# Optimization experiments

Hardware: AMD Instinct MI355X
Metric: run time of the kernel (lower is better)

The kernel has to match this reference:

```python
import math
import jax, jax.numpy as jnp
import numpy as np

B, H, L = 8, 512, 4096
N = 64 // 2  # d_state//2 complex pairs
DT_MIN, DT_MAX = 1e-3, 0.1


def setup_inputs() -> dict:
    key = jax.random.key(0)
    k_u, k_dt, k_C, k_D, k_W = jax.random.split(key, 5)
    u = jax.random.normal(k_u, (B, H, L), dtype=jnp.float32)
    log_dt = jax.random.uniform(k_dt, (H,), dtype=jnp.float32) * (
        math.log(DT_MAX) - math.log(DT_MIN)) + math.log(DT_MIN)
    log_A_real = jnp.log(0.5 * jnp.ones((H, N), dtype=jnp.float32))
    A_imag = math.pi * jnp.broadcast_to(jnp.arange(N, dtype=jnp.float32), (H, N))
    C = jax.random.normal(k_C, (H, N, 2), dtype=jnp.float32)  # view_as_real of cfloat
    D = jax.random.normal(k_D, (H,), dtype=jnp.float32)
    W_out = jax.random.normal(k_W, (2 * H, H), dtype=jnp.float32) * 0.05  # 1x1 conv weight
    b_out = jnp.zeros((2 * H,), dtype=jnp.float32)
    return {"u": u, "log_dt": log_dt, "log_A_real": log_A_real, "A_imag": A_imag,
            "C": C, "D": D, "W_out": W_out, "b_out": b_out}


def _ssm_kernel(log_dt, log_A_real, A_imag, C, length):
    dt = jnp.exp(log_dt)                             # (H,)
    A = -jnp.exp(log_A_real) + 1j * A_imag           # (H,N) complex
    dtA = A * dt[:, None]                            # (H,N)
    l = jnp.arange(length, dtype=jnp.float32)
    K = jnp.exp(dtA[:, :, None] * l)                 # (H,N,L) complex Vandermonde
    Cc = C[..., 0] + 1j * C[..., 1]                  # (H,N)
    Cs = Cc * (jnp.exp(dtA) - 1.0) / A               # (H,N)
    return 2.0 * jnp.einsum('hn,hnl->hl', Cs, K).real  # (H,L) real kernel


def reference(u, log_dt, log_A_real, A_imag, C, D, W_out, b_out):
    length = u.shape[-1]
    k = _ssm_kernel(log_dt, log_A_real, A_imag, C, length)  # (H,L)
    n_fft = 2 * length
    k_f = jnp.fft.rfft(k, n=n_fft)                   # (H, L+1)
    u_f = jnp.fft.rfft(u, n=n_fft)                   # (B,H,L+1)
    y = jnp.fft.irfft(u_f * k_f, n=n_fft)[..., :length]  # FFT convolution
    y = y + u * D[:, None]                           # D skip connection
    y = jax.nn.gelu(y, approximate=False)            # torch nn.GELU = exact erf
    y = jnp.einsum('oh,bhl->bol', W_out, y) + b_out[:, None]  # 1x1 conv
    a, b = jnp.split(y, 2, axis=-2)                  # GLU over channel dim
    return a * jax.nn.sigmoid(b)
```

## Files before the change

### kernel.cpp

```cpp
#include <hip/hip_runtime.h>
#include <math.h>

constexpr int cB = 8, cH = 512, cL = 4096, cN = 32;
constexpr int cG = 32, cLC = 128;
constexpr int cHN = cH * cN;

constexpr size_t OF_RR  = 0;
constexpr size_t OF_RI  = (size_t)cHN;
constexpr size_t OF_RPR = (size_t)2*cHN;
constexpr size_t OF_RPI = (size_t)3*cHN;
constexpr size_t OF_C2R = (size_t)4*cHN;
constexpr size_t OF_C2I = (size_t)5*cHN;
constexpr size_t OF_DR  = (size_t)6*cHN;
constexpr size_t OF_DI  = (size_t)7*cHN;
constexpr size_t OF_K   = (size_t)8*cHN;
constexpr size_t OF_WP  = OF_K + (size_t)512*128;
constexpr size_t OF_A   = OF_WP + (size_t)1024*512/2;
constexpr size_t OF_V   = OF_A + (size_t)512*128*192/2;
constexpr size_t OF_XP  = OF_V + (size_t)512*64*128/2;
constexpr size_t OF_G   = OF_XP + (size_t)512*256*64/2;

typedef __bf16 bf16x8 __attribute__((ext_vector_type(8)));
typedef float  f32x4  __attribute__((ext_vector_type(4)));

static __device__ __forceinline__ ushort f2bf(float x) {
    unsigned u = __float_as_uint(x);
    unsigned r = (u + 0x7fffu + ((u >> 16) & 1u)) >> 16;
    return (ushort)r;
}
static __device__ __forceinline__ float bf2f(ushort v) {
    return __uint_as_float(((unsigned)v) << 16);
}
static __device__ __forceinline__ unsigned pk2(float a, float b) {
    return (unsigned)f2bf(a) | ((unsigned)f2bf(b) << 16);
}
static __device__ __forceinline__ float gelu(float v) {
    return 0.5f * v * (1.0f + erff(v * 0.70710678118654752f));
}

__global__ void k_consts(const float* __restrict__ log_dt,
                         const float* __restrict__ log_A_real,
                         const float* __restrict__ A_imag,
                         const float* __restrict__ Cin,
                         float* __restrict__ ws)
{
    int tid = blockIdx.x * 256 + threadIdx.x;
    if (tid >= cHN) return;
    int h = tid >> 5;
    float dt = expf(log_dt[h]);
    float Ar = -expf(log_A_real[tid]);
    float Ai = A_imag[tid];
    float dr = dt * Ar, di = dt * Ai;
    float er = expf(dr);
    float rr = er * cosf(di), ri = er * sinf(di);
    float erL = expf(dr * (float)cLC);
    float diL = di * (float)cLC;
    float rpr = erL * cosf(diL), rpi = erL * sinf(diL);
    float cr = Cin[2*tid], ci = Cin[2*tid+1];
    float nr = rr - 1.0f, ni = ri;
    float inv = 1.0f / (Ar*Ar + Ai*Ai);
    float wr = (nr*Ar + ni*Ai) * inv;
    float wi = (ni*Ar - nr*Ai) * inv;
    float csr = cr*wr - ci*wi;
    float csi = cr*wi + ci*wr;
    ws[OF_RR  + tid] = rr;  ws[OF_RI  + tid] = ri;
    ws[OF_RPR + tid] = rpr; ws[OF_RPI + tid] = rpi;
    ws[OF_C2R + tid] = 2.0f*csr; ws[OF_C2I + tid] = 2.0f*csi;
    ws[OF_DR  + tid] = dr;  ws[OF_DI  + tid] = di;
}

__global__ void k_pack_w(const float* __restrict__ W, ushort* __restrict__ Wp)
{
    int idx = blockIdx.x * 256 + threadIdx.x;
    int base = idx * 4;
    int m = base >> 9;
    int k = base & 511;
    int src = (m & 1) ? (512 + (m >> 1)) : (m >> 1);
    float4 v = *(const float4*)&W[(size_t)src * 512 + k];
    ushort4 o;
    o.x = f2bf(v.x); o.y = f2bf(v.y); o.z = f2bf(v.z); o.w = f2bf(v.w);
    *(ushort4*)&Wp[base] = o;
}

__global__ void k_vmat(const float* __restrict__ ws, ushort* __restrict__ wsu)
{
    int tid = blockIdx.x * 256 + threadIdx.x;
    int h = tid >> 5, n = tid & 31;
    float dr = ws[OF_DR + tid], di = ws[OF_DI + tid];
    float e127 = expf(dr * 127.f), a127 = di * 127.f;
    float pr = e127 * cosf(a127), pi_ = e127 * sinf(a127);
    float rie = expf(-dr);
    float rc = rie * cosf(di), rs = -rie * sinf(di);
    ushort* vre = wsu + 2*OF_V + ((size_t)h*64 + n) * 128;
    ushort* vim = wsu + 2*OF_V + ((size_t)h*64 + 32 + n) * 128;
    for (int j4 = 0; j4 < 128; j4 += 4) {
        ushort4 r4, i4;
        #pragma unroll
        for (int e = 0; e < 4; ++e) {
            ((ushort*)&r4)[e] = f2bf(pr);
            ((ushort*)&i4)[e] = f2bf(pi_);
            float npr = pr*rc - pi_*rs;
            float npi = pr*rs + pi_*rc;
            pr = npr; pi_ = npi;
        }
        *(ushort4*)&vre[j4] = r4;
        *(ushort4*)&vim[j4] = i4;
    }
}

__global__ void k_emat(const float* __restrict__ ws, float* __restrict__ wsf,
                       ushort* __restrict__ wsu)
{
    int tid = blockIdx.x * 256 + threadIdx.x;
    int h = tid >> 7, l = tid & 127;
    float fl = (float)l, fl1 = (float)(l + 1);
    const float* dr_ = ws + OF_DR + (size_t)h*32;
    const float* di_ = ws + OF_DI + (size_t)h*32;
    const float* c2r_ = ws + OF_C2R + (size_t)h*32;
    const float* c2i_ = ws + OF_C2I + (size_t)h*32;
    ushort* rowA = wsu + 2*OF_A + ((size_t)h*128 + l) * 192;
    float kacc = 0.f;
    for (int n4 = 0; n4 < 32; n4 += 4) {
        ushort4 prq, npq;
        #pragma unroll
        for (int e = 0; e < 4; ++e) {
            int n = n4 + e;
            float dr = dr_[n], di = di_[n], c2r = c2r_[n], c2i = c2i_[n];
            float e0 = expf(dr * fl), a0 = di * fl;
            float c0 = cosf(a0), s0 = sinf(a0);
            kacc += e0 * (c2r*c0 - c2i*s0);
            float e1 = expf(dr * fl1), a1 = di * fl1;
            float c1 = cosf(a1), s1 = sinf(a1);
            ((ushort*)&prq)[e] = f2bf(e1 * (c2r*c1 - c2i*s1));
            ((ushort*)&npq)[e] = f2bf(-e1 * (c2r*s1 + c2i*c1));
        }
        *(ushort4*)&rowA[128 + n4] = prq;
        *(ushort4*)&rowA[160 + n4] = npq;
    }
    wsf[OF_K + (size_t)h*128 + l] = kacc;
}

__global__ void k_build_T(const float* __restrict__ wsf, const float* __restrict__ Dvec,
                          ushort* __restrict__ wsu)
{
    __shared__ float kv[256];
    int t = threadIdx.x;
    int tid = blockIdx.x * 256 + t;
    int h = tid >> 7, l = tid & 127;
    kv[t] = wsf[OF_K + (size_t)blockIdx.x * 256 + t];
    __syncthreads();
    const float* krow = kv + ((t >> 7) << 7);
    float Dh = Dvec[h];
    ushort* row = wsu + 2*OF_A + ((size_t)h*128 + l) * 192;
    for (int j8 = 0; j8 < 128; j8 += 8) {
        uint4 q;
        unsigned w[4];
        #pragma unroll
        for (int p = 0; p < 4; ++p) {
            int j0 = j8 + 2*p, j1 = j0 + 1;
            float v0 = (j0 <= l) ? krow[l - j0] : 0.f;
            float v1 = (j1 <= l) ? krow[l - j1] : 0.f;
            if (j0 == l) v0 += Dh;
            if (j1 == l) v1 += Dh;
            w[p] = pk2(v0, v1);
        }
        q.x = w[0]; q.y = w[1]; q.z = w[2]; q.w = w[3];
        *(uint4*)&row[j8] = q;
    }
}

__global__ __launch_bounds__(256) void k_state_gemm(const float* __restrict__ u,
                                                    const ushort* __restrict__ wsu,
                                                    ushort* __restrict__ xp)
{
    __shared__ ushort Vs[64 * 136];
    __shared__ ushort Bs[256 * 40];
    const int t = threadIdx.x;
    const int h = blockIdx.x;
    const int wn = t >> 6, lane = t & 63;
    const int lm = lane & 15, q = lane >> 4;

    {
        int idx = t * 32;
        int row = idx >> 7, kk = idx & 127;
        const ushort* src = wsu + 2*OF_V + ((size_t)h*64 + row) * 128 + kk;
        uint4 v0 = *(const uint4*)&src[0],  v1 = *(const uint4*)&src[8];
        uint4 v2 = *(const uint4*)&src[16], v3 = *(const uint4*)&src[24];
        ushort* d = (ushort*)Vs + row * 136 + kk;
        *(uint4*)&d[0] = v0; *(uint4*)&d[8] = v1;
        *(uint4*)&d[16] = v2; *(uint4*)&d[24] = v3;
    }

    const int b = t >> 5, c = t & 31;
    f32x4 acc[4][4];
    #pragma unroll
    for (int i = 0; i < 4; ++i)
        #pragma unroll
        for (int j = 0; j < 4; ++j) acc[i][j] = (f32x4){0.f,0.f,0.f,0.f};

    for (int k0 = 0; k0 < 128; k0 += 32) {
        const float* up = u + ((size_t)(b*cH + h)) * cL + (size_t)c*128 + k0;
        float4 f[8];
        #pragma unroll
        for (int e = 0; e < 8; ++e) f[e] = *(const float4*)&up[4*e];
        __syncthreads();
        ushort* d = (ushort*)Bs + t * 40;
        #pragma unroll
        for (int e = 0; e < 4; ++e) {
            uint4 w;
            w.x = pk2(f[2*e].x, f[2*e].y);   w.y = pk2(f[2*e].z, f[2*e].w);
            w.z = pk2(f[2*e+1].x, f[2*e+1].y); w.w = pk2(f[2*e+1].z, f[2*e+1].w);
            *(uint4*)&d[8*e] = w;
        }
        __syncthreads();
        bf16x8 af[4], bfr[4];
        #pragma unroll
        for (int mi = 0; mi < 4; ++mi)
            af[mi] = *(const bf16x8*)&Vs[(16*mi + lm) * 136 + k0 + 8*q];
        #pragma unroll
        for (int ni = 0; ni < 4; ++ni)
            bfr[ni] = *(const bf16x8*)&Bs[(64*wn + 16*ni + lm) * 40 + 8*q];
        #pragma unroll
        for (int mi = 0; mi < 4; ++mi)
            #pragma unroll
            for (int ni = 0; ni < 4; ++ni)
                acc[mi][ni] = __builtin_amdgcn_mfma_f32_16x16x32_bf16(af[mi], bfr[ni], acc[mi][ni], 0,0,0);
    }
    #pragma unroll
    for (int mi = 0; mi < 4; ++mi)
        #pragma unroll
        for (int ni = 0; ni < 4; ++ni) {
            int col = 64*wn + 16*ni + lm;
            int comp = 16*mi + 4*q;
            ushort4 st;
            st.x = f2bf(acc[mi][ni][0]); st.y = f2bf(acc[mi][ni][1]);
            st.z = f2bf(acc[mi][ni][2]); st.w = f2bf(acc[mi][ni][3]);
            *(ushort4*)&xp[((size_t)h*256 + col) * 64 + comp] = st;
        }
}

__global__ __launch_bounds__(256) void k_scan2(const float* __restrict__ ws,
                                               ushort* __restrict__ xp)
{
    int tid = blockIdx.x * 256 + threadIdx.x;
    int n  = tid & 31;
    int bh = tid >> 5;
    int h  = bh & (cH - 1);
    int b  = bh >> 9;
    float rpr = ws[OF_RPR + (size_t)h*32 + n];
    float rpi = ws[OF_RPI + (size_t)h*32 + n];
    float Xr = 0.f, Xi = 0.f;
    ushort* base = xp + ((size_t)h*256 + (size_t)b*32) * 64 + n;
    for (int c = 0; c < cG; ++c) {
        ushort* p = base + (size_t)c * 64;
        float sr = bf2f(p[0]), si = bf2f(p[32]);
        p[0]  = f2bf(Xr);
        p[32] = f2bf(Xi);
        float nXr = fmaf(rpr, Xr, fmaf(-rpi, Xi, sr));
        float nXi = fmaf(rpr, Xi, fmaf(rpi, Xr, si));
        Xr = nXr; Xi = nXi;
    }
}

__global__ __launch_bounds__(256) void k_conv(const float* __restrict__ u,
                                              const ushort* __restrict__ wsu,
                                              ushort* __restrict__ g)
{
    __shared__ ushort As[128 * 40];
    __shared__ ushort Bs[128 * 40];
    const int t = threadIdx.x;
    const int ctile = blockIdx.x;
    const int h = blockIdx.y;
    const int wave = t >> 6, lane = t & 63;
    const int wm = wave & 1, wn = wave >> 1;
    const int lm = lane & 15, q = lane >> 4;

    const int arow = t & 127, ah = t >> 7;
    const int col = arow, half = ah;
    const int gc = ctile * 128 + col;
    const int ub = gc >> 5, uc = gc & 31;

    const ushort* Ab = wsu + 2*OF_A + ((size_t)h*128 + arow) * 192;
    const ushort* xpB = wsu + 2*OF_XP + ((size_t)h*256 + gc) * 64;

    f32x4 acc[4][4];
    #pragma unroll
    for (int i = 0; i < 4; ++i)
        #pragma unroll
        for (int j = 0; j < 4; ++j) acc[i][j] = (f32x4){0.f,0.f,0.f,0.f};

    for (int k0 = 0; k0 < 192; k0 += 32) {
        uint4 a0 = *(const uint4*)&Ab[k0 + 16*ah];
        uint4 a1 = *(const uint4*)&Ab[k0 + 16*ah + 8];
        uint4 b0, b1;
        if (k0 < 128) {
            const float* up = u + ((size_t)(ub*cH + h)) * cL + (size_t)uc*128 + k0 + 16*half;
            float4 f0 = *(const float4*)&up[0],  f1 = *(const float4*)&up[4];
            float4 f2 = *(const float4*)&up[8],  f3 = *(const float4*)&up[12];
            b0.x = pk2(f0.x,f0.y); b0.y = pk2(f0.z,f0.w);
            b0.z = pk2(f1.x,f1.y); b0.w = pk2(f1.z,f1.w);
            b1.x = pk2(f2.x,f2.y); b1.y = pk2(f2.z,f2.w);
            b1.z = pk2(f3.x,f3.y); b1.w = pk2(f3.z,f3.w);
        } else {
            const ushort* xs = xpB + (k0 - 128) + 16*half;
            b0 = *(const uint4*)&xs[0];
            b1 = *(const uint4*)&xs[8];
        }
        __syncthreads();
        *(uint4*)&As[arow*40 + 16*ah]     = a0;
        *(uint4*)&As[arow*40 + 16*ah + 8] = a1;
        *(uint4*)&Bs[col*40 + 16*half]     = b0;
        *(uint4*)&Bs[col*40 + 16*half + 8] = b1;
        __syncthreads();
        bool skip = (wm == 0) && (k0 == 64 || k0 == 96);
        if (!skip) {
            bf16x8 af[4], bfr[4];
            #pragma unroll
            for (int mi = 0; mi < 4; ++mi)
                af[mi] = *(const bf16x8*)&As[(64*wm + 16*mi + lm) * 40 + 8*q];
            #pragma unroll
            for (int ni = 0; ni < 4; ++ni)
                bfr[ni] = *(const bf16x8*)&Bs[(64*wn + 16*ni + lm) * 40 + 8*q];
            #pragma unroll
            for (int mi = 0; mi < 4; ++mi)
                #pragma unroll
                for (int ni = 0; ni < 4; ++ni)
                    acc[mi][ni] = __builtin_amdgcn_mfma_f32_16x16x32_bf16(af[mi], bfr[ni], acc[mi][ni], 0,0,0);
        }
    }
    #pragma unroll
    for (int ni = 0; ni < 4; ++ni) {
        int ocol = ctile*128 + 64*wn + 16*ni + lm;
        int ob = ocol >> 5, oc = ocol & 31;
        ushort* grow = g + ((size_t)(ob*cH + h)) * cL + (size_t)oc*128;
        #pragma unroll
        for (int mi = 0; mi < 4; ++mi) {
            int l = 64*wm + 16*mi + 4*q;
            ushort4 st;
            st.x = f2bf(gelu(acc[mi][ni][0]));
            st.y = f2bf(gelu(acc[mi][ni][1]));
            st.z = f2bf(gelu(acc[mi][ni][2]));
            st.w = f2bf(gelu(acc[mi][ni][3]));
            *(ushort4*)&grow[l] = st;
        }
    }
}

constexpr int LDK = 40;
__global__ __launch_bounds__(256) void k_gemm_mfma(const ushort* __restrict__ Wp,
                                                   const float* __restrict__ bias,
                                                   const ushort* __restrict__ gbf,
                                                   float* __restrict__ out)
{
    __shared__ ushort As[128 * LDK];
    __shared__ ushort Bs[128 * LDK];
    const int t    = threadIdx.x;
    const int l0   = blockIdx.x * 128;
    const int by   = blockIdx.y;
    const int b    = blockIdx.z;
    const int wave = t >> 6, lane = t & 63;
    const int wm   = wave & 1, wn = wave >> 1;
    const int lm   = lane & 15, q = lane >> 4;

    const int arow = t & 127;
    const int ah   = t >> 7;
    const int lq = t & 15, kp = t >> 4;
    const int ko = kp >> 2;
    const int kr = (2 * kp) & 7;

    const ushort* gB = gbf + (size_t)b * ((size_t)cH * cL);
    const ushort* wRow = Wp + (size_t)(by * 128 + arow) * 512 + ah * 16;

    f32x4 acc[4][4];
    #pragma unroll
    for (int i = 0; i < 4; ++i)
        #pragma unroll
        for (int j = 0; j < 4; ++j)
            acc[i][j] = (f32x4){0.f, 0.f, 0.f, 0.f};

    for (int k0 = 0; k0 < cH; k0 += 32) {
        uint4 wa0 = *(const uint4*)&wRow[k0];
        uint4 wa1 = *(const uint4*)&wRow[k0 + 8];
        uint4 g0  = *(const uint4*)&gB[(size_t)(k0 + 2*kp)     * cL + l0 + 8*lq];
        uint4 g1  = *(const uint4*)&gB[(size_t)(k0 + 2*kp + 1) * cL + l0 + 8*lq];
        __syncthreads();
        *(uint4*)&As[arow * LDK + 16*ah]     = wa0;
        *(uint4*)&As[arow * LDK + 16*ah + 8] = wa1;
        {
            unsigned ua[4] = {g0.x, g0.y, g0.z, g0.w};
            unsigned ub[4] = {g1.x, g1.y, g1.z, g1.w};
            #pragma unroll
            for (int e = 0; e < 4; ++e) {
                unsigned w0 = (ua[e] & 0xffffu) | (ub[e] << 16);
                unsigned w1 = (ua[e] >> 16)     | (ub[e] & 0xffff0000u);
                int lr0 = 8*lq + 2*e;
                int c0  = ((ko ^ (lq & 3)) << 3) + kr;
                *(unsigned*)&Bs[lr0 * LDK + c0]       = w0;
                *(unsigned*)&Bs[(lr0 + 1) * LDK + c0] = w1;
            }
        }
        __syncthreads();
        bf16x8 af[4], bf[4];
        #pragma unroll
        for (int mi = 0; mi < 4; ++mi) {
            int row = 64*wm + 16*mi + lm;
            af[mi] = *(const bf16x8*)&As[row * LDK + (q << 3)];
        }
        #pragma unroll
        for (int ni = 0; ni < 4; ++ni) {
            int row = 64*wn + 16*ni + lm;
            int kx  = (row >> 3) & 3;
            bf[ni] = *(const bf16x8*)&Bs[row * LDK + ((q ^ kx) << 3)];
        }
        #pragma unroll
        for (int mi = 0; mi < 4; ++mi)
            #pragma unroll
            for (int ni = 0; ni < 4; ++ni)
                acc[mi][ni] = __builtin_amdgcn_mfma_f32_16x16x32_bf16(af[mi], bf[ni], acc[mi][ni], 0, 0, 0);
    }

    const int obase = by * 64 + 32 * wm;
    #pragma unroll
    for (int mi = 0; mi < 4; ++mi) {
        #pragma unroll
        for (int p = 0; p < 2; ++p) {
            int o = obase + 8*mi + 2*q + p;
            float ba = bias[o], bb = bias[512 + o];
            float* orow = out + ((size_t)b * cH + o) * cL + l0 + 64*wn + lm;
            #pragma unroll
            for (int ni = 0; ni < 4; ++ni) {
                float av = acc[mi][ni][2*p]     + ba;
                float gv = acc[mi][ni][2*p + 1] + bb;
                orow[16 * ni] = av / (1.f + expf(-gv));
            }
        }
    }
}

extern "C" void kernel_launch(void* const* d_in, const int* in_sizes, int n_in,
                              void* d_out, int out_size, void* d_ws, size_t ws_size,
                              hipStream_t stream)
{
    (void)in_sizes; (void)n_in; (void)out_size; (void)ws_size;
    const float* u          = (const float*)d_in[0];
    const float* log_dt     = (const float*)d_in[1];
    const float* log_A_real = (const float*)d_in[2];
    const float* A_imag     = (const float*)d_in[3];
    const float* C          = (const float*)d_in[4];
    const float* D          = (const float*)d_in[5];
    const float* W          = (const float*)d_in[6];
    const float* bias       = (const float*)d_in[7];
    float* out = (float*)d_out;
    float* ws  = (float*)d_ws;
    ushort* wsu = (ushort*)d_ws;
    ushort* Wp  = wsu + 2*OF_WP;
    ushort* xp  = wsu + 2*OF_XP;
    ushort* gbf = wsu + 2*OF_G;

    hipLaunchKernelGGL(k_consts, dim3(cHN/256), dim3(256), 0, stream,
                       log_dt, log_A_real, A_imag, C, ws);
    hipLaunchKernelGGL(k_pack_w, dim3(1024*512/4/256), dim3(256), 0, stream, W, Wp);
    hipLaunchKernelGGL(k_vmat, dim3(cHN/256), dim3(256), 0, stream, ws, wsu);
    hipLaunchKernelGGL(k_emat, dim3(512*128/256), dim3(256), 0, stream, ws, ws, wsu);
    hipLaunchKernelGGL(k_build_T, dim3(512*128/256), dim3(256), 0, stream, ws, D, wsu);
    hipLaunchKernelGGL(k_state_gemm, dim3(512), dim3(256), 0, stream, u, wsu, xp);
    hipLaunchKernelGGL(k_scan2, dim3(cB*cH*cN/256), dim3(256), 0, stream, ws, xp);
    hipLaunchKernelGGL(k_conv, dim3(2, 512), dim3(256), 0, stream, u, wsu, gbf);
    hipLaunchKernelGGL(k_gemm_mfma, dim3(cL/128, 1024/128, cB), dim3(256), 0, stream,
                       Wp, bias, gbf, out);
}
```

Baseline: 297.7 us.

## Transpose GELU output and double-buffer GEMM tiles with direct global-to-LDS loads

Adds a transpose kernel that writes the GELU output in (b, l, h) layout so both GEMM operands are K-contiguous. The output GEMM is rewritten to stage tiles with global_load_lds directly into double-buffered LDS, overlapping the next tile's loads with MFMA on the current one and dropping the register shuffle used for the B operand. The cost is an extra kernel pass that reads and writes the whole bf16 activation tensor (about 32 MB each way), and a transposed buffer that reuses the OF_A workspace region. The new LDS tiles are unpadded, which may cause bank conflicts.

```diff
diff --git a/kernel.cpp b/kernel.cpp
--- a/kernel.cpp
+++ b/kernel.cpp
@@ -19,6 +19,7 @@
 constexpr size_t OF_V   = OF_A + (size_t)512*128*192/2;
 constexpr size_t OF_XP  = OF_V + (size_t)512*64*128/2;
 constexpr size_t OF_G   = OF_XP + (size_t)512*256*64/2;
+constexpr size_t OF_GT  = OF_A;
 
 typedef __bf16 bf16x8 __attribute__((ext_vector_type(8)));
 typedef float  f32x4  __attribute__((ext_vector_type(4)));
@@ -36,6 +37,11 @@
 }
 static __device__ __forceinline__ float gelu(float v) {
     return 0.5f * v * (1.0f + erff(v * 0.70710678118654752f));
+}
+static __device__ __forceinline__ void gload16(const void* g, void* l) {
+    __builtin_amdgcn_global_load_lds(
+        (const __attribute__((address_space(1))) unsigned*)g,
+        (__attribute__((address_space(3))) unsigned*)l, 16, 0, 0);
 }
 
 __global__ void k_consts(const float* __restrict__ log_dt,
@@ -346,14 +352,47 @@
     }
 }
 
-constexpr int LDK = 40;
-__global__ __launch_bounds__(256) void k_gemm_mfma(const ushort* __restrict__ Wp,
-                                                   const float* __restrict__ bias,
-                                                   const ushort* __restrict__ gbf,
-                                                   float* __restrict__ out)
-{
-    __shared__ ushort As[128 * LDK];
-    __shared__ ushort Bs[128 * LDK];
+__global__ __launch_bounds__(256) void k_transpose(const ushort* __restrict__ gsrc,
+                                                   ushort* __restrict__ gT)
+{
+    __shared__ ushort tile[64 * 64];
+    const int t = threadIdx.x;
+    const int b  = blockIdx.z;
+    const int h0 = blockIdx.y << 6;
+    const int l0 = blockIdx.x << 6;
+    const ushort* gb = gsrc + ((size_t)b * cH + h0) * cL + l0;
+    const int lb = t & 7;
+    #pragma unroll
+    for (int half = 0; half < 2; ++half) {
+        int r = (t >> 3) + half * 32;
+        uint4 v = *(const uint4*)&gb[(size_t)r * cL + lb * 8];
+        int sb = lb ^ (r & 7) ^ (r >> 3);
+        *(uint4*)&tile[r * 64 + sb * 8] = v;
+    }
+    __syncthreads();
+    ushort* gTb = gT + ((size_t)b * cL + l0) * cH + h0;
+    #pragma unroll
+    for (int half = 0; half < 2; ++half) {
+        int l  = (t >> 3) + half * 32;
+        int hb = t & 7;
+        ushort vals[8];
+        #pragma unroll
+        for (int e = 0; e < 8; ++e) {
+            int r  = hb * 8 + e;
+            int sb = (l >> 3) ^ (r & 7) ^ (r >> 3);
+            vals[e] = tile[r * 64 + sb * 8 + (l & 7)];
+        }
+        *(uint4*)&gTb[(size_t)l * cH + hb * 8] = *(uint4*)vals;
+    }
+}
+
+__global__ __launch_bounds__(256) void k_gemm2(const ushort* __restrict__ Wp,
+                                               const float* __restrict__ bias,
+                                               const ushort* __restrict__ gT,
+                                               float* __restrict__ out)
+{
+    __shared__ ushort As[2][128 * 32];
+    __shared__ ushort Bs[2][128 * 32];
     const int t    = threadIdx.x;
     const int l0   = blockIdx.x * 128;
     const int by   = blockIdx.y;
@@ -362,14 +401,10 @@
     const int wm   = wave & 1, wn = wave >> 1;
     const int lm   = lane & 15, q = lane >> 4;
 
-    const int arow = t & 127;
-    const int ah   = t >> 7;
-    const int lq = t & 15, kp = t >> 4;
-    const int ko = kp >> 2;
-    const int kr = (2 * kp) & 7;
-
-    const ushort* gB = gbf + (size_t)b * ((size_t)cH * cL);
-    const ushort* wRow = Wp + (size_t)(by * 128 + arow) * 512 + ah * 16;
+    const int srow = lane >> 2;
+    const int scol = (lane & 3) * 8;
+    const ushort* Ag = Wp + (size_t)(by * 128) * 512;
+    const ushort* Bg = gT + ((size_t)b * cL + l0) * 512;
 
     f32x4 acc[4][4];
     #pragma unroll
@@ -378,46 +413,41 @@
         for (int j = 0; j < 4; ++j)
             acc[i][j] = (f32x4){0.f, 0.f, 0.f, 0.f};
 
-    for (int k0 = 0; k0 < cH; k0 += 32) {
-        uint4 wa0 = *(const uint4*)&wRow[k0];
-        uint4 wa1 = *(const uint4*)&wRow[k0 + 8];
-        uint4 g0  = *(const uint4*)&gB[(size_t)(k0 + 2*kp)     * cL + l0 + 8*lq];
-        uint4 g1  = *(const uint4*)&gB[(size_t)(k0 + 2*kp + 1) * cL + l0 + 8*lq];
-        __syncthreads();
-        *(uint4*)&As[arow * LDK + 16*ah]     = wa0;
-        *(uint4*)&As[arow * LDK + 16*ah + 8] = wa1;
-        {
-            unsigned ua[4] = {g0.x, g0.y, g0.z, g0.w};
-            unsigned ub[4] = {g1.x, g1.y, g1.z, g1.w};
-            #pragma unroll
-            for (int e = 0; e < 4; ++e) {
-                unsigned w0 = (ua[e] & 0xffffu) | (ub[e] << 16);
-                unsigned w1 = (ua[e] >> 16)     | (ub[e] & 0xffff0000u);
-                int lr0 = 8*lq + 2*e;
-                int c0  = ((ko ^ (lq & 3)) << 3) + kr;
-                *(unsigned*)&Bs[lr0 * LDK + c0]       = w0;
-                *(unsigned*)&Bs[(lr0 + 1) * LDK + c0] = w1;
-            }
-        }
-        __syncthreads();
-        bf16x8 af[4], bf[4];
-        #pragma unroll
-        for (int mi = 0; mi < 4; ++mi) {
-            int row = 64*wm + 16*mi + lm;
-            af[mi] = *(const bf16x8*)&As[row * LDK + (q << 3)];
-        }
-        #pragma unroll
-        for (int ni = 0; ni < 4; ++ni) {
-            int row = 64*wn + 16*ni + lm;
-            int kx  = (row >> 3) & 3;
-            bf[ni] = *(const bf16x8*)&Bs[row * LDK + ((q ^ kx) << 3)];
-        }
+    auto stage = [&](ushort* Asb, ushort* Bsb, int k0) {
+        #pragma unroll
+        for (int j = 0; j < 2; ++j) {
+            int row = 32*wave + 16*j + srow;
+            gload16(Ag + (size_t)row * 512 + k0 + scol,
+                    (char*)Asb + wave*2048 + j*1024);
+            gload16(Bg + (size_t)row * 512 + k0 + scol,
+                    (char*)Bsb + wave*2048 + j*1024);
+        }
+    };
+    auto compute = [&](const ushort* Asb, const ushort* Bsb) {
+        bf16x8 af[4], bfr[4];
+        #pragma unroll
+        for (int mi = 0; mi < 4; ++mi)
+            af[mi] = *(const bf16x8*)&Asb[(64*wm + 16*mi + lm) * 32 + 8*q];
+        #pragma unroll
+        for (int ni = 0; ni < 4; ++ni)
+            bfr[ni] = *(const bf16x8*)&Bsb[(64*wn + 16*ni + lm) * 32 + 8*q];
         #pragma unroll
         for (int mi = 0; mi < 4; ++mi)
             #pragma unroll
             for (int ni = 0; ni < 4; ++ni)
-                acc[mi][ni] = __builtin_amdgcn_mfma_f32_16x16x32_bf16(af[mi], bf[ni], acc[mi][ni], 0, 0, 0);
-    }
+                acc[mi][ni] = __builtin_amdgcn_mfma_f32_16x16x32_bf16(af[mi], bfr[ni], acc[mi][ni], 0,0,0);
+    };
+
+    stage(As[0], Bs[0], 0);
+    __syncthreads();
+    int cur = 0;
+    for (int ks = 0; ks < 15; ++ks) {
+        stage(As[cur ^ 1], Bs[cur ^ 1], (ks + 1) * 32);
+        compute(As[cur], Bs[cur]);
+        __syncthreads();
+        cur ^= 1;
+    }
+    compute(As[cur], Bs[cur]);
 
     const int obase = by * 64 + 32 * wm;
     #pragma unroll
@@ -456,6 +486,7 @@
     ushort* Wp  = wsu + 2*OF_WP;
     ushort* xp  = wsu + 2*OF_XP;
     ushort* gbf = wsu + 2*OF_G;
+    ushort* gTu = wsu + 2*OF_GT;
 
     hipLaunchKernelGGL(k_consts, dim3(cHN/256), dim3(256), 0, stream,
                        log_dt, log_A_real, A_imag, C, ws);
@@ -466,6 +497,7 @@
     hipLaunchKernelGGL(k_state_gemm, dim3(512), dim3(256), 0, stream, u, wsu, xp);
     hipLaunchKernelGGL(k_scan2, dim3(cB*cH*cN/256), dim3(256), 0, stream, ws, xp);
     hipLaunchKernelGGL(k_conv, dim3(2, 512), dim3(256), 0, stream, u, wsu, gbf);
-    hipLaunchKernelGGL(k_gemm_mfma, dim3(cL/128, 1024/128, cB), dim3(256), 0, stream,
-                       Wp, bias, gbf, out);
-}
+    hipLaunchKernelGGL(k_transpose, dim3(cL/64, cH/64, cB), dim3(256), 0, stream, gbf, gTu);
+    hipLaunchKernelGGL(k_gemm2, dim3(cL/128, 1024/128, cB), dim3(256), 0, stream,
+                       Wp, bias, gTu, out);
+}
```

Result: faster. 290.9 us (-2.3%).
